# Performance work log

Measured on AMD Instinct MI355X. Metric: run time of the kernel, lower is better.

## Reference

```python
import jax, jax.numpy as jnp
import numpy as np


def setup_inputs() -> dict:
    key = jax.random.key(0)
    k1, k2 = jax.random.split(key)
    pred_pts = jax.random.normal(k1, (8, 3, 4096), dtype=jnp.float32)  # [B,3,N]
    gt_pts = jax.random.normal(k2, (8, 4096, 3), dtype=jnp.float32)    # [B,M,3]
    return {"pred_pts": pred_pts, "gt_pts": gt_pts}


def _chamfer(p, g):
    # p: [B,N,3], g: [B,M,3]
    # squared euclidean distance matrix via ||p||^2 + ||g||^2 - 2 p.g
    pn = jnp.sum(p * p, axis=-1)  # [B,N]
    gn = jnp.sum(g * g, axis=-1)  # [B,M]
    cross = jnp.einsum("bnd,bmd->bnm", p, g)  # [B,N,M]
    D = pn[:, :, None] + gn[:, None, :] - 2.0 * cross  # [B,N,M]
    dist1 = jnp.min(D, axis=2)  # [B,N] min over gt for each pred point
    dist2 = jnp.min(D, axis=1)  # [B,M] min over pred for each gt point
    return dist1, dist2


def reference(pred_pts, gt_pts):
    p = jnp.swapaxes(pred_pts, -2, -1).astype(jnp.float32)  # [B,N,3]
    g = gt_pts  # [B,M,3]
    dist1, dist2 = _chamfer(p, g)
    per_batch = jnp.mean(dist1, axis=1) + jnp.mean(dist2, axis=1)  # [B]
    loss = jnp.sum(per_batch) / gt_pts.shape[0]
    return loss
```

## Files before the change

### kernel.cpp

```cpp
#include <hip/hip_runtime.h>

#define NPTS 4096
#define BATCH 8
#define BLK 256
#define P 4
#define CHUNK 512
#define NCHUNK (NPTS / CHUNK)
#define OWN_PER_BLK (BLK * P)
#define OWN_BLKS (NPTS / OWN_PER_BLK)
#define BLOCKS_PER_PASS (BATCH * OWN_BLKS * NCHUNK)
#define TOTAL_BLOCKS (2 * BLOCKS_PER_PASS)
#define HALF_OWN (BATCH * NPTS)
#define TOTAL_OWN (2 * HALF_OWN)
#define COMBINE_BLOCKS (TOTAL_OWN / BLK)

__global__ __launch_bounds__(BLK) void chamfer_partial_kernel(
    const float* __restrict__ pred,
    const float* __restrict__ gt,
    float* __restrict__ partial)
{
    __shared__ float4 s[CHUNK];

    const int bid  = blockIdx.x;
    const int pass = bid / BLOCKS_PER_PASS;
    int r = bid - pass * BLOCKS_PER_PASS;
    const int c = r % NCHUNK;
    r /= NCHUNK;
    const int b = r / OWN_BLKS;
    const int j = r - b * OWN_BLKS;
    const int t = threadIdx.x;

    const float* p = pred + (size_t)b * 3 * NPTS;
    const float* g = gt   + (size_t)b * NPTS * 3;
    const int cbase = c * CHUNK;

    if (pass == 0) {
        for (int i = t; i < CHUNK; i += BLK) {
            int gi = cbase + i;
            float gx = g[gi * 3 + 0], gy = g[gi * 3 + 1], gz = g[gi * 3 + 2];
            s[i] = make_float4(-2.f * gx, -2.f * gy, -2.f * gz,
                               fmaf(gx, gx, fmaf(gy, gy, gz * gz)));
        }
    } else {
        for (int i = t; i < CHUNK; i += BLK) {
            int pi = cbase + i;
            float px = p[pi], py = p[NPTS + pi], pz = p[2 * NPTS + pi];
            s[i] = make_float4(-2.f * px, -2.f * py, -2.f * pz,
                               fmaf(px, px, fmaf(py, py, pz * pz)));
        }
    }

    float x[P], y[P], z[P], n2[P];
    #pragma unroll
    for (int k = 0; k < P; ++k) {
        int idx = j * OWN_PER_BLK + k * BLK + t;
        if (pass == 0) {
            x[k] = p[idx]; y[k] = p[NPTS + idx]; z[k] = p[2 * NPTS + idx];
        } else {
            x[k] = g[idx * 3 + 0]; y[k] = g[idx * 3 + 1]; z[k] = g[idx * 3 + 2];
        }
        n2[k] = fmaf(x[k], x[k], fmaf(y[k], y[k], z[k] * z[k]));
    }
    __syncthreads();

    float ma[P], mb_[P];
    #pragma unroll
    for (int k = 0; k < P; ++k) { ma[k] = 3.4e38f; mb_[k] = 3.4e38f; }

    #pragma unroll 2
    for (int mm = 0; mm < CHUNK; mm += 4) {
        float4 q0 = s[mm + 0];
        float4 q1 = s[mm + 1];
        float4 q2 = s[mm + 2];
        float4 q3 = s[mm + 3];
        #pragma unroll
        for (int k = 0; k < P; ++k) {
            ma[k]  = fminf(ma[k],  fmaf(x[k], q0.x, fmaf(y[k], q0.y, fmaf(z[k], q0.z, q0.w))));
            mb_[k] = fminf(mb_[k], fmaf(x[k], q1.x, fmaf(y[k], q1.y, fmaf(z[k], q1.z, q1.w))));
            ma[k]  = fminf(ma[k],  fmaf(x[k], q2.x, fmaf(y[k], q2.y, fmaf(z[k], q2.z, q2.w))));
            mb_[k] = fminf(mb_[k], fmaf(x[k], q3.x, fmaf(y[k], q3.y, fmaf(z[k], q3.z, q3.w))));
        }
    }

    #pragma unroll
    for (int k = 0; k < P; ++k) {
        int idx = j * OWN_PER_BLK + k * BLK + t;
        int o = pass * HALF_OWN + b * NPTS + idx;
        partial[(size_t)c * TOTAL_OWN + o] = n2[k] + fminf(ma[k], mb_[k]);
    }
}

__global__ __launch_bounds__(BLK) void chamfer_combine_kernel(
    const float* __restrict__ partial, float* __restrict__ bsum)
{
    __shared__ float red[BLK / 64];
    const int t = threadIdx.x;
    const int o = blockIdx.x * BLK + t;
    float v = 3.4e38f;
    #pragma unroll
    for (int c = 0; c < NCHUNK; ++c)
        v = fminf(v, partial[(size_t)c * TOTAL_OWN + o]);
    #pragma unroll
    for (int off = 32; off > 0; off >>= 1)
        v += __shfl_down(v, off, 64);
    if ((t & 63) == 0) red[t >> 6] = v;
    __syncthreads();
    if (t == 0) bsum[blockIdx.x] = red[0] + red[1] + red[2] + red[3];
}

__global__ __launch_bounds__(COMBINE_BLOCKS) void chamfer_final_kernel(
    const float* __restrict__ bsum, float* __restrict__ out)
{
    __shared__ float red[COMBINE_BLOCKS / 64];
    const int t = threadIdx.x;
    float v = bsum[t];
    #pragma unroll
    for (int off = 32; off > 0; off >>= 1)
        v += __shfl_down(v, off, 64);
    if ((t & 63) == 0) red[t >> 6] = v;
    __syncthreads();
    if (t == 0) {
        float s = 0.f;
        #pragma unroll
        for (int w = 0; w < COMBINE_BLOCKS / 64; ++w) s += red[w];
        out[0] = s * (1.0f / ((float)NPTS * (float)BATCH));
    }
}

extern "C" void kernel_launch(void* const* d_in, const int* in_sizes, int n_in,
                              void* d_out, int out_size, void* d_ws, size_t ws_size,
                              hipStream_t stream) {
    const float* pred = (const float*)d_in[0];
    const float* gt   = (const float*)d_in[1];
    float* out = (float*)d_out;

    float* partial = (float*)d_ws;
    float* bsum    = partial + (size_t)NCHUNK * TOTAL_OWN;

    chamfer_partial_kernel<<<TOTAL_BLOCKS, BLK, 0, stream>>>(pred, gt, partial);
    chamfer_combine_kernel<<<COMBINE_BLOCKS, BLK, 0, stream>>>(partial, bsum);
    chamfer_final_kernel<<<1, COMBINE_BLOCKS, 0, stream>>>(bsum, out);
}
```

Before: 32.15 us.

## Use packed f32x2 FMA/min for chamfer inner loop and retile to P=8

Rewrites the distance inner loop to operate on pairs of owned points using 2-wide float vectors, so the compiler can emit packed FP32 FMA and min instructions (v_pk_fma_f32) and halve the ALU instruction count. It also doubles the points owned per thread to 8 and halves the gt chunk to 256, which doubles the number of chunks and partial writes while keeping the block count constant. The risks are higher register pressure, the cost of splatting shared values into pairs, and a combine pass that now reads 16 partials per output instead of 8.

```diff
diff --git a/kernel.cpp b/kernel.cpp
--- a/kernel.cpp
+++ b/kernel.cpp
@@ -1,10 +1,13 @@
 #include <hip/hip_runtime.h>
+
+typedef float f32x2 __attribute__((ext_vector_type(2)));
 
 #define NPTS 4096
 #define BATCH 8
 #define BLK 256
-#define P 4
-#define CHUNK 512
+#define P 8
+#define NPAIR (P / 2)
+#define CHUNK 256
 #define NCHUNK (NPTS / CHUNK)
 #define OWN_PER_BLK (BLK * P)
 #define OWN_BLKS (NPTS / OWN_PER_BLK)
@@ -13,6 +16,10 @@
 #define HALF_OWN (BATCH * NPTS)
 #define TOTAL_OWN (2 * HALF_OWN)
 #define COMBINE_BLOCKS (TOTAL_OWN / BLK)
+
+static __device__ __forceinline__ f32x2 splat2(float v) {
+    f32x2 r; r.x = v; r.y = v; return r;
+}
 
 __global__ __launch_bounds__(BLK) void chamfer_partial_kernel(
     const float* __restrict__ pred,
@@ -34,15 +41,14 @@
     const float* g = gt   + (size_t)b * NPTS * 3;
     const int cbase = c * CHUNK;
 
-    if (pass == 0) {
-        for (int i = t; i < CHUNK; i += BLK) {
+    {
+        int i = t;
+        if (pass == 0) {
             int gi = cbase + i;
             float gx = g[gi * 3 + 0], gy = g[gi * 3 + 1], gz = g[gi * 3 + 2];
             s[i] = make_float4(-2.f * gx, -2.f * gy, -2.f * gz,
                                fmaf(gx, gx, fmaf(gy, gy, gz * gz)));
-        }
-    } else {
-        for (int i = t; i < CHUNK; i += BLK) {
+        } else {
             int pi = cbase + i;
             float px = p[pi], py = p[NPTS + pi], pz = p[2 * NPTS + pi];
             s[i] = make_float4(-2.f * px, -2.f * py, -2.f * pz,
@@ -50,43 +56,56 @@
         }
     }
 
-    float x[P], y[P], z[P], n2[P];
+    f32x2 X[NPAIR], Y[NPAIR], Z[NPAIR], N2[NPAIR];
     #pragma unroll
     for (int k = 0; k < P; ++k) {
         int idx = j * OWN_PER_BLK + k * BLK + t;
+        float x, y, z;
         if (pass == 0) {
-            x[k] = p[idx]; y[k] = p[NPTS + idx]; z[k] = p[2 * NPTS + idx];
+            x = p[idx]; y = p[NPTS + idx]; z = p[2 * NPTS + idx];
         } else {
-            x[k] = g[idx * 3 + 0]; y[k] = g[idx * 3 + 1]; z[k] = g[idx * 3 + 2];
+            x = g[idx * 3 + 0]; y = g[idx * 3 + 1]; z = g[idx * 3 + 2];
         }
-        n2[k] = fmaf(x[k], x[k], fmaf(y[k], y[k], z[k] * z[k]));
+        X[k >> 1][k & 1] = x;
+        Y[k >> 1][k & 1] = y;
+        Z[k >> 1][k & 1] = z;
+        N2[k >> 1][k & 1] = fmaf(x, x, fmaf(y, y, z * z));
     }
     __syncthreads();
 
-    float ma[P], mb_[P];
+    f32x2 A[NPAIR], B[NPAIR];
     #pragma unroll
-    for (int k = 0; k < P; ++k) { ma[k] = 3.4e38f; mb_[k] = 3.4e38f; }
+    for (int pk = 0; pk < NPAIR; ++pk) { A[pk] = splat2(3.4e38f); B[pk] = splat2(3.4e38f); }
 
     #pragma unroll 2
-    for (int mm = 0; mm < CHUNK; mm += 4) {
+    for (int mm = 0; mm < CHUNK; mm += 2) {
         float4 q0 = s[mm + 0];
         float4 q1 = s[mm + 1];
-        float4 q2 = s[mm + 2];
-        float4 q3 = s[mm + 3];
+        f32x2 q0x = splat2(q0.x), q0y = splat2(q0.y), q0z = splat2(q0.z), q0w = splat2(q0.w);
+        f32x2 q1x = splat2(q1.x), q1y = splat2(q1.y), q1z = splat2(q1.z), q1w = splat2(q1.w);
         #pragma unroll
-        for (int k = 0; k < P; ++k) {
-            ma[k]  = fminf(ma[k],  fmaf(x[k], q0.x, fmaf(y[k], q0.y, fmaf(z[k], q0.z, q0.w))));
-            mb_[k] = fminf(mb_[k], fmaf(x[k], q1.x, fmaf(y[k], q1.y, fmaf(z[k], q1.z, q1.w))));
-            ma[k]  = fminf(ma[k],  fmaf(x[k], q2.x, fmaf(y[k], q2.y, fmaf(z[k], q2.z, q2.w))));
-            mb_[k] = fminf(mb_[k], fmaf(x[k], q3.x, fmaf(y[k], q3.y, fmaf(z[k], q3.z, q3.w))));
+        for (int pk = 0; pk < NPAIR; ++pk) {
+            f32x2 d0 = __builtin_elementwise_fma(X[pk], q0x,
+                        __builtin_elementwise_fma(Y[pk], q0y,
+                         __builtin_elementwise_fma(Z[pk], q0z, q0w)));
+            A[pk] = __builtin_elementwise_min(A[pk], d0);
+            f32x2 d1 = __builtin_elementwise_fma(X[pk], q1x,
+                        __builtin_elementwise_fma(Y[pk], q1y,
+                         __builtin_elementwise_fma(Z[pk], q1z, q1w)));
+            B[pk] = __builtin_elementwise_min(B[pk], d1);
         }
     }
 
     #pragma unroll
-    for (int k = 0; k < P; ++k) {
-        int idx = j * OWN_PER_BLK + k * BLK + t;
-        int o = pass * HALF_OWN + b * NPTS + idx;
-        partial[(size_t)c * TOTAL_OWN + o] = n2[k] + fminf(ma[k], mb_[k]);
+    for (int pk = 0; pk < NPAIR; ++pk) {
+        f32x2 mn = __builtin_elementwise_min(A[pk], B[pk]);
+        #pragma unroll
+        for (int h = 0; h < 2; ++h) {
+            int k = 2 * pk + h;
+            int idx = j * OWN_PER_BLK + k * BLK + t;
+            int o = pass * HALF_OWN + b * NPTS + idx;
+            partial[(size_t)c * TOTAL_OWN + o] = N2[pk][h] + mn[h];
+        }
     }
 }
 
```

After: 33.42 us. 1.04x slower.

## Use packed f32x2 FMA/min with double-buffered LDS register prefetch

Applied to the files above, without the earlier changes.

Cuts the points owned per thread from 4 to 2 and stores them as 2-wide float vectors, so the inner distance loop can map to packed FMA and min instructions. Shared-memory reads are double-buffered into register arrays of 8 float4 each, prefetching the next group while the current one computes. The LDS array is padded so the prefetch can run past the chunk end, and launch bounds request 4 blocks per SM. Halving P doubles the grid, so each gt/pred chunk is staged into LDS twice as often. It also relies on the compiler actually emitting packed math.

```diff
diff --git a/kernel.cpp b/kernel.cpp
--- a/kernel.cpp
+++ b/kernel.cpp
@@ -1,9 +1,11 @@
 #include <hip/hip_runtime.h>
+
+typedef float f32x2 __attribute__((ext_vector_type(2)));
 
 #define NPTS 4096
 #define BATCH 8
 #define BLK 256
-#define P 4
+#define P 2
 #define CHUNK 512
 #define NCHUNK (NPTS / CHUNK)
 #define OWN_PER_BLK (BLK * P)
@@ -14,12 +16,16 @@
 #define TOTAL_OWN (2 * HALF_OWN)
 #define COMBINE_BLOCKS (TOTAL_OWN / BLK)
 
-__global__ __launch_bounds__(BLK) void chamfer_partial_kernel(
+static __device__ __forceinline__ f32x2 splat2(float v) {
+    f32x2 r; r.x = v; r.y = v; return r;
+}
+
+__global__ __launch_bounds__(BLK, 4) void chamfer_partial_kernel(
     const float* __restrict__ pred,
     const float* __restrict__ gt,
     float* __restrict__ partial)
 {
-    __shared__ float4 s[CHUNK];
+    __shared__ float4 s[CHUNK + 16];
 
     const int bid  = blockIdx.x;
     const int pass = bid / BLOCKS_PER_PASS;
@@ -34,15 +40,15 @@
     const float* g = gt   + (size_t)b * NPTS * 3;
     const int cbase = c * CHUNK;
 
-    if (pass == 0) {
-        for (int i = t; i < CHUNK; i += BLK) {
+    #pragma unroll
+    for (int u = 0; u < CHUNK / BLK; ++u) {
+        int i = u * BLK + t;
+        if (pass == 0) {
             int gi = cbase + i;
             float gx = g[gi * 3 + 0], gy = g[gi * 3 + 1], gz = g[gi * 3 + 2];
             s[i] = make_float4(-2.f * gx, -2.f * gy, -2.f * gz,
                                fmaf(gx, gx, fmaf(gy, gy, gz * gz)));
-        }
-    } else {
-        for (int i = t; i < CHUNK; i += BLK) {
+        } else {
             int pi = cbase + i;
             float px = p[pi], py = p[NPTS + pi], pz = p[2 * NPTS + pi];
             s[i] = make_float4(-2.f * px, -2.f * py, -2.f * pz,
@@ -50,43 +56,57 @@
         }
     }
 
-    float x[P], y[P], z[P], n2[P];
+    f32x2 X, Y, Z, N2;
     #pragma unroll
     for (int k = 0; k < P; ++k) {
         int idx = j * OWN_PER_BLK + k * BLK + t;
+        float x, y, z;
         if (pass == 0) {
-            x[k] = p[idx]; y[k] = p[NPTS + idx]; z[k] = p[2 * NPTS + idx];
+            x = p[idx]; y = p[NPTS + idx]; z = p[2 * NPTS + idx];
         } else {
-            x[k] = g[idx * 3 + 0]; y[k] = g[idx * 3 + 1]; z[k] = g[idx * 3 + 2];
+            x = g[idx * 3 + 0]; y = g[idx * 3 + 1]; z = g[idx * 3 + 2];
         }
-        n2[k] = fmaf(x[k], x[k], fmaf(y[k], y[k], z[k] * z[k]));
+        X[k] = x; Y[k] = y; Z[k] = z;
+        N2[k] = fmaf(x, x, fmaf(y, y, z * z));
     }
     __syncthreads();
 
-    float ma[P], mb_[P];
+    f32x2 A = splat2(3.4e38f), B = splat2(3.4e38f);
+
+    float4 q0[8], q1[8];
     #pragma unroll
-    for (int k = 0; k < P; ++k) { ma[k] = 3.4e38f; mb_[k] = 3.4e38f; }
+    for (int u = 0; u < 8; ++u) q0[u] = s[u];
 
     #pragma unroll 2
-    for (int mm = 0; mm < CHUNK; mm += 4) {
-        float4 q0 = s[mm + 0];
-        float4 q1 = s[mm + 1];
-        float4 q2 = s[mm + 2];
-        float4 q3 = s[mm + 3];
+    for (int mm = 0; mm < CHUNK; mm += 16) {
         #pragma unroll
-        for (int k = 0; k < P; ++k) {
-            ma[k]  = fminf(ma[k],  fmaf(x[k], q0.x, fmaf(y[k], q0.y, fmaf(z[k], q0.z, q0.w))));
-            mb_[k] = fminf(mb_[k], fmaf(x[k], q1.x, fmaf(y[k], q1.y, fmaf(z[k], q1.z, q1.w))));
-            ma[k]  = fminf(ma[k],  fmaf(x[k], q2.x, fmaf(y[k], q2.y, fmaf(z[k], q2.z, q2.w))));
-            mb_[k] = fminf(mb_[k], fmaf(x[k], q3.x, fmaf(y[k], q3.y, fmaf(z[k], q3.z, q3.w))));
+        for (int u = 0; u < 8; ++u) q1[u] = s[mm + 8 + u];
+        #pragma unroll
+        for (int u = 0; u < 8; ++u) {
+            f32x2 d = __builtin_elementwise_fma(X, splat2(q0[u].x),
+                       __builtin_elementwise_fma(Y, splat2(q0[u].y),
+                        __builtin_elementwise_fma(Z, splat2(q0[u].z), splat2(q0[u].w))));
+            if (u & 1) B = __builtin_elementwise_min(B, d);
+            else       A = __builtin_elementwise_min(A, d);
+        }
+        #pragma unroll
+        for (int u = 0; u < 8; ++u) q0[u] = s[mm + 16 + u];
+        #pragma unroll
+        for (int u = 0; u < 8; ++u) {
+            f32x2 d = __builtin_elementwise_fma(X, splat2(q1[u].x),
+                       __builtin_elementwise_fma(Y, splat2(q1[u].y),
+                        __builtin_elementwise_fma(Z, splat2(q1[u].z), splat2(q1[u].w))));
+            if (u & 1) B = __builtin_elementwise_min(B, d);
+            else       A = __builtin_elementwise_min(A, d);
         }
     }
 
+    f32x2 mn = __builtin_elementwise_min(A, B);
     #pragma unroll
     for (int k = 0; k < P; ++k) {
         int idx = j * OWN_PER_BLK + k * BLK + t;
         int o = pass * HALF_OWN + b * NPTS + idx;
-        partial[(size_t)c * TOTAL_OWN + o] = n2[k] + fminf(ma[k], mb_[k]);
+        partial[(size_t)c * TOTAL_OWN + o] = N2[k] + mn[k];
     }
 }
 
```

After: 35.60 us. 10.7% more time.

## Have each block own all points with 64-point staged tiles

Applied to the files above, without the earlier changes.

Reorganizes the partial kernel so each block keeps all 4096 owned points in registers (16 per thread) and stages only 64 query points in shared memory, giving 64 slots per batch and pass. The inner loop merges two distances per min, and the squared-norm term is computed at the end instead of being held in registers. This raises register-level reuse of owned points and shrinks shared-memory staging. In exchange, the partial buffer grows eightfold and the combine kernel must reduce 64 slots. Every block also reloads the full point set from global memory, which adds a lot of memory traffic.

```diff
diff --git a/kernel.cpp b/kernel.cpp
--- a/kernel.cpp
+++ b/kernel.cpp
@@ -3,90 +3,72 @@
 #define NPTS 4096
 #define BATCH 8
 #define BLK 256
-#define P 4
-#define CHUNK 512
-#define NCHUNK (NPTS / CHUNK)
-#define OWN_PER_BLK (BLK * P)
-#define OWN_BLKS (NPTS / OWN_PER_BLK)
-#define BLOCKS_PER_PASS (BATCH * OWN_BLKS * NCHUNK)
+#define P 16
+#define STG 64
+#define SLOTS (NPTS / STG)
+#define BLOCKS_PER_PASS (BATCH * SLOTS)
 #define TOTAL_BLOCKS (2 * BLOCKS_PER_PASS)
 #define HALF_OWN (BATCH * NPTS)
 #define TOTAL_OWN (2 * HALF_OWN)
 #define COMBINE_BLOCKS (TOTAL_OWN / BLK)
 
-__global__ __launch_bounds__(BLK) void chamfer_partial_kernel(
+__global__ __launch_bounds__(BLK, 4) void chamfer_partial_kernel(
     const float* __restrict__ pred,
     const float* __restrict__ gt,
     float* __restrict__ partial)
 {
-    __shared__ float4 s[CHUNK];
+    __shared__ float4 s[STG];
 
     const int bid  = blockIdx.x;
-    const int pass = bid / BLOCKS_PER_PASS;
-    int r = bid - pass * BLOCKS_PER_PASS;
-    const int c = r % NCHUNK;
-    r /= NCHUNK;
-    const int b = r / OWN_BLKS;
-    const int j = r - b * OWN_BLKS;
-    const int t = threadIdx.x;
+    const int pass = bid >> 9;
+    const int r    = bid & 511;
+    const int b    = r >> 6;
+    const int c    = r & 63;
+    const int t    = threadIdx.x;
 
     const float* p = pred + (size_t)b * 3 * NPTS;
     const float* g = gt   + (size_t)b * NPTS * 3;
-    const int cbase = c * CHUNK;
 
-    if (pass == 0) {
-        for (int i = t; i < CHUNK; i += BLK) {
-            int gi = cbase + i;
-            float gx = g[gi * 3 + 0], gy = g[gi * 3 + 1], gz = g[gi * 3 + 2];
-            s[i] = make_float4(-2.f * gx, -2.f * gy, -2.f * gz,
-                               fmaf(gx, gx, fmaf(gy, gy, gz * gz)));
-        }
-    } else {
-        for (int i = t; i < CHUNK; i += BLK) {
-            int pi = cbase + i;
-            float px = p[pi], py = p[NPTS + pi], pz = p[2 * NPTS + pi];
-            s[i] = make_float4(-2.f * px, -2.f * py, -2.f * pz,
-                               fmaf(px, px, fmaf(py, py, pz * pz)));
-        }
+    if (t < STG) {
+        int i = c * STG + t;
+        float qx, qy, qz;
+        if (pass == 0) { qx = g[i * 3 + 0]; qy = g[i * 3 + 1]; qz = g[i * 3 + 2]; }
+        else           { qx = p[i]; qy = p[NPTS + i]; qz = p[2 * NPTS + i]; }
+        s[t] = make_float4(-2.f * qx, -2.f * qy, -2.f * qz,
+                           fmaf(qx, qx, fmaf(qy, qy, qz * qz)));
     }
 
-    float x[P], y[P], z[P], n2[P];
+    float x[P], y[P], z[P];
     #pragma unroll
     for (int k = 0; k < P; ++k) {
-        int idx = j * OWN_PER_BLK + k * BLK + t;
-        if (pass == 0) {
-            x[k] = p[idx]; y[k] = p[NPTS + idx]; z[k] = p[2 * NPTS + idx];
-        } else {
-            x[k] = g[idx * 3 + 0]; y[k] = g[idx * 3 + 1]; z[k] = g[idx * 3 + 2];
-        }
-        n2[k] = fmaf(x[k], x[k], fmaf(y[k], y[k], z[k] * z[k]));
+        int idx = k * BLK + t;
+        if (pass == 0) { x[k] = p[idx]; y[k] = p[NPTS + idx]; z[k] = p[2 * NPTS + idx]; }
+        else           { x[k] = g[idx * 3 + 0]; y[k] = g[idx * 3 + 1]; z[k] = g[idx * 3 + 2]; }
     }
     __syncthreads();
 
-    float ma[P], mb_[P];
+    float acc[P];
     #pragma unroll
-    for (int k = 0; k < P; ++k) { ma[k] = 3.4e38f; mb_[k] = 3.4e38f; }
+    for (int k = 0; k < P; ++k) acc[k] = 3.4e38f;
 
     #pragma unroll 2
-    for (int mm = 0; mm < CHUNK; mm += 4) {
-        float4 q0 = s[mm + 0];
-        float4 q1 = s[mm + 1];
-        float4 q2 = s[mm + 2];
-        float4 q3 = s[mm + 3];
+    for (int ss = 0; ss < STG; ss += 2) {
+        float4 q0 = s[ss + 0];
+        float4 q1 = s[ss + 1];
         #pragma unroll
         for (int k = 0; k < P; ++k) {
-            ma[k]  = fminf(ma[k],  fmaf(x[k], q0.x, fmaf(y[k], q0.y, fmaf(z[k], q0.z, q0.w))));
-            mb_[k] = fminf(mb_[k], fmaf(x[k], q1.x, fmaf(y[k], q1.y, fmaf(z[k], q1.z, q1.w))));
-            ma[k]  = fminf(ma[k],  fmaf(x[k], q2.x, fmaf(y[k], q2.y, fmaf(z[k], q2.z, q2.w))));
-            mb_[k] = fminf(mb_[k], fmaf(x[k], q3.x, fmaf(y[k], q3.y, fmaf(z[k], q3.z, q3.w))));
+            float d0 = fmaf(x[k], q0.x, fmaf(y[k], q0.y, fmaf(z[k], q0.z, q0.w)));
+            float d1 = fmaf(x[k], q1.x, fmaf(y[k], q1.y, fmaf(z[k], q1.z, q1.w)));
+            acc[k] = fminf(fminf(d0, d1), acc[k]);
         }
     }
 
     #pragma unroll
     for (int k = 0; k < P; ++k) {
-        int idx = j * OWN_PER_BLK + k * BLK + t;
+        int idx = k * BLK + t;
         int o = pass * HALF_OWN + b * NPTS + idx;
-        partial[(size_t)c * TOTAL_OWN + o] = n2[k] + fminf(ma[k], mb_[k]);
+        float n2 = fmaf(x[k], x[k], fmaf(y[k], y[k], z[k] * z[k]));
+        partial[(size_t)c * TOTAL_OWN + o] = n2 + acc[k];
     }
 }
 
@@ -97,9 +79,9 @@
     const int t = threadIdx.x;
     const int o = blockIdx.x * BLK + t;
     float v = 3.4e38f;
-    #pragma unroll
-    for (int c = 0; c < NCHUNK; ++c)
-        v = fminf(v, partial[(size_t)c * TOTAL_OWN + o]);
+    #pragma unroll 8
+    for (int cc = 0; cc < SLOTS; ++cc)
+        v = fminf(v, partial[(size_t)cc * TOTAL_OWN + o]);
     #pragma unroll
     for (int off = 32; off > 0; off >>= 1)
         v += __shfl_down(v, off, 64);
@@ -135,7 +117,7 @@
     float* out = (float*)d_out;
 
     float* partial = (float*)d_ws;
-    float* bsum    = partial + (size_t)NCHUNK * TOTAL_OWN;
+    float* bsum    = partial + (size_t)SLOTS * TOTAL_OWN;
 
     chamfer_partial_kernel<<<TOTAL_BLOCKS, BLK, 0, stream>>>(pred, gt, partial);
     chamfer_combine_kernel<<<COMBINE_BLOCKS, BLK, 0, stream>>>(partial, bsum);
```

Result: slower. 47.71 us (+48.4%).
